# Kernel tuning notes

Hardware: AMD Instinct MI355X
Metric: run time of the kernel (lower is better)

The kernel has to match this reference:

```python
import jax, jax.numpy as jnp
import numpy as np

N = 100_000      # nodes
E = 1_600_000    # edges (before self loops)
IN, HID, OUT, H = 128, 32, 40, 4
NEG_SLOPE = 0.2  # PyG GATConv default


def setup_inputs() -> dict:
    key = jax.random.key(0)
    ks = jax.random.split(key, 10)
    s = 0.1  # small init scale (glorot-like)
    return {
        "x": jax.random.normal(ks[0], (N, IN), jnp.float32),
        "edge_index": jax.random.randint(ks[1], (2, E), 0, N, dtype=jnp.int32),
        "W1": jax.random.normal(ks[2], (IN, H * HID), jnp.float32) * s,
        "att_src1": jax.random.normal(ks[3], (H, HID), jnp.float32) * s,
        "att_dst1": jax.random.normal(ks[4], (H, HID), jnp.float32) * s,
        "b1": jnp.zeros((H * HID,), jnp.float32),
        "W2": jax.random.normal(ks[5], (H * HID, H * OUT), jnp.float32) * s,
        "att_src2": jax.random.normal(ks[6], (H, OUT), jnp.float32) * s,
        "att_dst2": jax.random.normal(ks[7], (H, OUT), jnp.float32) * s,
        "b2": jnp.zeros((OUT,), jnp.float32),
    }


def gat_layer(x, src, dst, W, a_src, a_dst, b, concat):
    """PyG-style GATConv: edge (src -> dst), softmax over incoming edges per dst."""
    Hh, C = a_src.shape
    h = (x @ W).reshape(-1, Hh, C)                      # [N, H, C]
    s_src = jnp.einsum('nhc,hc->nh', h, a_src)           # [N, H]
    s_dst = jnp.einsum('nhc,hc->nh', h, a_dst)           # [N, H]
    e = jax.nn.leaky_relu(s_src[src] + s_dst[dst], NEG_SLOPE)  # [E', H]
    m = jax.ops.segment_max(e, dst, num_segments=N)      # per-dst max for stability
    p = jnp.exp(e - m[dst])
    z = jax.ops.segment_sum(p, dst, num_segments=N)
    alpha = p / z[dst]                                    # segment softmax [E', H]
    out = jax.ops.segment_sum(alpha[:, :, None] * h[src], dst, num_segments=N)  # [N,H,C]
    out = out.reshape(-1, Hh * C) if concat else out.mean(axis=1)
    return out + b


def reference(x, edge_index, W1, att_src1, att_dst1, b1, W2, att_src2, att_dst2, b2):
    loops = jnp.arange(N, dtype=edge_index.dtype)        # PyG add_self_loops=True
    src = jnp.concatenate([edge_index[0], loops])
    dst = jnp.concatenate([edge_index[1], loops])
    h = jax.nn.elu(gat_layer(x, src, dst, W1, att_src1, att_dst1, b1, concat=True))
    h = gat_layer(h, src, dst, W2, att_src2, att_dst2, b2, concat=False)
    return jax.nn.log_softmax(h, axis=1)
```

## Files before the change

### kernel.cpp

```cpp
#include <hip/hip_runtime.h>
#include <hip/hip_bf16.h>

#define N_NODES 100000
#define M_PAD   100096
#define N_EDGES 1600000
#define E_TOT   (N_EDGES + N_NODES)
#define NEG_SLOPE 0.2f

#define G_NODES 128
#define BUCKETS ((N_NODES + G_NODES - 1) / G_NODES)
#define REP 512
#define SLICE ((E_TOT + REP - 1) / REP)

typedef __attribute__((ext_vector_type(8))) short s16x8;
typedef __attribute__((ext_vector_type(4))) float f32x4;
typedef __attribute__((ext_vector_type(2))) float f32x2;

__device__ __forceinline__ float lo16(unsigned u) { return __uint_as_float(u << 16); }
__device__ __forceinline__ float hi16(unsigned u) { return __uint_as_float(u & 0xffff0000u); }

__device__ __forceinline__ short f2bf(float f) {
    __hip_bfloat16 b = __float2bfloat16(f);
    return *(short*)&b;
}


__global__ __launch_bounds__(256) void slice_count_kernel(const int* __restrict__ ei,
                                                          int* __restrict__ cnt) {
    __shared__ int h[BUCKETS];
    for (int i = threadIdx.x; i < BUCKETS; i += 256) h[i] = 0;
    __syncthreads();
    int r = blockIdx.x;
    int lo = r * SLICE, hi = min(lo + SLICE, E_TOT);
    for (int e = lo + threadIdx.x; e < hi; e += 256) {
        int d = (e < N_EDGES) ? ei[N_EDGES + e] : e - N_EDGES;
        atomicAdd(&h[d >> 7], 1);
    }
    __syncthreads();
    for (int i = threadIdx.x; i < BUCKETS; i += 256)
        cnt[(size_t)r * BUCKETS + i] = h[i];
}

__global__ __launch_bounds__(REP) void col_scan_kernel(int* __restrict__ cnt,
                                                       int* __restrict__ bsum) {
    __shared__ int lds[REP];
    int b = blockIdx.x, tid = threadIdx.x;
    int v = cnt[(size_t)tid * BUCKETS + b];
    lds[tid] = v;
    __syncthreads();
    for (int off = 1; off < REP; off <<= 1) {
        int t = (tid >= off) ? lds[tid - off] : 0;
        __syncthreads();
        lds[tid] += t;
        __syncthreads();
    }
    cnt[(size_t)tid * BUCKETS + b] = lds[tid] - v;
    if (tid == REP - 1) bsum[b] = lds[tid];
}

__global__ __launch_bounds__(1024) void bucket_scan_kernel(const int* __restrict__ bsum,
                                                           int* __restrict__ boff) {
    __shared__ int lds[1024];
    int tid = threadIdx.x;
    int v = (tid < BUCKETS) ? bsum[tid] : 0;
    lds[tid] = v;
    __syncthreads();
    for (int off = 1; off < 1024; off <<= 1) {
        int t = (tid >= off) ? lds[tid - off] : 0;
        __syncthreads();
        lds[tid] += t;
        __syncthreads();
    }
    if (tid < BUCKETS) boff[tid] = lds[tid] - v;
    if (tid == 0) boff[BUCKETS] = E_TOT;
}

__global__ __launch_bounds__(256) void bucket_scatter_kernel(const int* __restrict__ ei,
                                                             const int* __restrict__ colx,
                                                             const int* __restrict__ boff,
                                                             int2* __restrict__ tmp) {
    __shared__ int lcur[BUCKETS];
    int r = blockIdx.x;
    for (int i = threadIdx.x; i < BUCKETS; i += 256)
        lcur[i] = boff[i] + colx[(size_t)r * BUCKETS + i];
    __syncthreads();
    int lo = r * SLICE, hi = min(lo + SLICE, E_TOT);
    for (int e = lo + threadIdx.x; e < hi; e += 256) {
        int s, d;
        if (e < N_EDGES) { s = ei[e]; d = ei[N_EDGES + e]; }
        else             { s = d = e - N_EDGES; }
        int pos = atomicAdd(&lcur[d >> 7], 1);
        tmp[pos] = make_int2(s, d);
    }
}

__global__ __launch_bounds__(256) void bucket_build_kernel(const int2* __restrict__ tmp,
                                                           const int* __restrict__ boff,
                                                           int* __restrict__ rowptr,
                                                           int* __restrict__ csr) {
    __shared__ int hcnt[G_NODES];
    __shared__ int hoff[G_NODES];
    int b = blockIdx.x;
    int base = boff[b], cnt = boff[b + 1] - base;
    int tid = threadIdx.x;
    if (tid < G_NODES) hcnt[tid] = 0;
    __syncthreads();
    for (int i = tid; i < cnt; i += 256)
        atomicAdd(&hcnt[tmp[base + i].y & (G_NODES - 1)], 1);
    __syncthreads();
    if (tid < G_NODES) hoff[tid] = hcnt[tid];
    __syncthreads();
    for (int off = 1; off < G_NODES; off <<= 1) {
        int t = (tid < G_NODES && tid >= off) ? hoff[tid - off] : 0;
        __syncthreads();
        if (tid < G_NODES) hoff[tid] += t;
        __syncthreads();
    }
    if (tid < G_NODES) {
        int excl = hoff[tid] - hcnt[tid];
        int node = b * G_NODES + tid;
        if (node < N_NODES) rowptr[node] = base + excl;
        hcnt[tid] = excl;
    }
    __syncthreads();
    for (int i = tid; i < cnt; i += 256) {
        int2 e = tmp[base + i];
        int pos = base + atomicAdd(&hcnt[e.y & (G_NODES - 1)], 1);
        csr[pos] = e.x;
    }
    if (b == 0 && tid == 0) rowptr[N_NODES] = E_TOT;
}


__global__ void cvt_w_kernel(const float* __restrict__ W1, __hip_bfloat16* __restrict__ W1t,
                             const float* __restrict__ W2, __hip_bfloat16* __restrict__ W2t) {
    int idx = blockIdx.x * blockDim.x + threadIdx.x;
    if (idx < 128 * 128) {
        int k = idx >> 7, n = idx & 127;
        W1t[n * 128 + k] = __float2bfloat16(W1[idx]);
    } else if (idx < 128 * 128 + 128 * 160) {
        int i = idx - 128 * 128;
        int k = i / 160, n = i - k * 160;
        W2t[n * 128 + k] = __float2bfloat16(W2[i]);
    }
}


template<int NCOLS>
__global__ __launch_bounds__(256) void mfma_gemm_f32a_kernel(const float* __restrict__ A,
                                                             const __hip_bfloat16* __restrict__ Bt,
                                                             unsigned char* __restrict__ Cq) {
    constexpr int CG = NCOLS / 32;
    int wid = threadIdx.x >> 6;
    int lane = threadIdx.x & 63;
    int wr = wid >> 1, wc = wid & 1;
    int l15 = lane & 15, lk = lane >> 4;

    s16x8 bfrag[CG][4];
    #pragma unroll
    for (int cg = 0; cg < CG; ++cg) {
        int col = wc * (NCOLS / 2) + cg * 16 + l15;
        #pragma unroll
        for (int ks = 0; ks < 4; ++ks)
            bfrag[cg][ks] = *(const s16x8*)&Bt[col * 128 + ks * 32 + lk * 8];
    }
    int rowblk = blockIdx.x * 128;
    #pragma unroll
    for (int st = 0; st < 4; ++st) {
        int rbase = rowblk + st * 32 + wr * 16;
        int row = rbase + l15;
        bool ok = row < N_NODES;
        s16x8 afrag[4];
        #pragma unroll
        for (int ks = 0; ks < 4; ++ks) {
            if (ok) {
                float4 a0 = *(const float4*)&A[(size_t)row * 128 + ks * 32 + lk * 8];
                float4 a1 = *(const float4*)&A[(size_t)row * 128 + ks * 32 + lk * 8 + 4];
                s16x8 af;
                af[0] = f2bf(a0.x); af[1] = f2bf(a0.y); af[2] = f2bf(a0.z); af[3] = f2bf(a0.w);
                af[4] = f2bf(a1.x); af[5] = f2bf(a1.y); af[6] = f2bf(a1.z); af[7] = f2bf(a1.w);
                afrag[ks] = af;
            } else {
                afrag[ks] = (s16x8){0,0,0,0,0,0,0,0};
            }
        }
        f32x4 acc[CG];
        #pragma unroll
        for (int cg = 0; cg < CG; ++cg) acc[cg] = (f32x4){0.f, 0.f, 0.f, 0.f};
        #pragma unroll
        for (int ks = 0; ks < 4; ++ks) {
            #pragma unroll
            for (int cg = 0; cg < CG; ++cg)
                acc[cg] = __builtin_amdgcn_mfma_f32_16x16x32_bf16(afrag[ks], bfrag[cg][ks], acc[cg], 0, 0, 0);
        }
        #pragma unroll
        for (int cg = 0; cg < CG; ++cg) {
            int c = wc * (NCOLS / 2) + cg * 16 + l15;
            unsigned w01 = __builtin_amdgcn_cvt_pk_fp8_f32(acc[cg][0], acc[cg][1], 0, false);
            unsigned w23 = __builtin_amdgcn_cvt_pk_fp8_f32(acc[cg][2], acc[cg][3], 0, false);
            size_t base = (size_t)(rbase + lk * 4) * NCOLS + c;
            Cq[base]             = (unsigned char)(w01 & 0xff);
            Cq[base + NCOLS]     = (unsigned char)((w01 >> 8) & 0xff);
            Cq[base + 2 * NCOLS] = (unsigned char)(w23 & 0xff);
            Cq[base + 3 * NCOLS] = (unsigned char)((w23 >> 8) & 0xff);
        }
    }
}


template<int NCOLS>
__global__ __launch_bounds__(256) void mfma_gemm_kernel(const __hip_bfloat16* __restrict__ A,
                                                        const __hip_bfloat16* __restrict__ Bt,
                                                        unsigned char* __restrict__ Cq) {
    constexpr int CG = NCOLS / 32;
    int wid = threadIdx.x >> 6;
    int lane = threadIdx.x & 63;
    int wr = wid >> 1, wc = wid & 1;
    int l15 = lane & 15, lk = lane >> 4;

    s16x8 bfrag[CG][4];
    #pragma unroll
    for (int cg = 0; cg < CG; ++cg) {
        int col = wc * (NCOLS / 2) + cg * 16 + l15;
        #pragma unroll
        for (int ks = 0; ks < 4; ++ks)
            bfrag[cg][ks] = *(const s16x8*)&Bt[col * 128 + ks * 32 + lk * 8];
    }
    int rowblk = blockIdx.x * 128;
    #pragma unroll
    for (int st = 0; st < 4; ++st) {
        int rbase = rowblk + st * 32 + wr * 16;
        s16x8 afrag[4];
        #pragma unroll
        for (int ks = 0; ks < 4; ++ks)
            afrag[ks] = *(const s16x8*)&A[(size_t)(rbase + l15) * 128 + ks * 32 + lk * 8];
        f32x4 acc[CG];
        #pragma unroll
        for (int cg = 0; cg < CG; ++cg) acc[cg] = (f32x4){0.f, 0.f, 0.f, 0.f};
        #pragma unroll
        for (int ks = 0; ks < 4; ++ks) {
            #pragma unroll
            for (int cg = 0; cg < CG; ++cg)
                acc[cg] = __builtin_amdgcn_mfma_f32_16x16x32_bf16(afrag[ks], bfrag[cg][ks], acc[cg], 0, 0, 0);
        }
        #pragma unroll
        for (int cg = 0; cg < CG; ++cg) {
            int c = wc * (NCOLS / 2) + cg * 16 + l15;
            unsigned w01 = __builtin_amdgcn_cvt_pk_fp8_f32(acc[cg][0], acc[cg][1], 0, false);
            unsigned w23 = __builtin_amdgcn_cvt_pk_fp8_f32(acc[cg][2], acc[cg][3], 0, false);
            size_t base = (size_t)(rbase + lk * 4) * NCOLS + c;
            Cq[base]             = (unsigned char)(w01 & 0xff);
            Cq[base + NCOLS]     = (unsigned char)((w01 >> 8) & 0xff);
            Cq[base + 2 * NCOLS] = (unsigned char)(w23 & 0xff);
            Cq[base + 3 * NCOLS] = (unsigned char)((w23 >> 8) & 0xff);
        }
    }
}


template<int C, int J>
__global__ void score_fp8_kernel(const unsigned char* __restrict__ hq,
                                 const float* __restrict__ att_src,
                                 const float* __restrict__ att_dst,
                                 float* __restrict__ s_src, float* __restrict__ s_dst, int n) {
    int idx = blockIdx.x * blockDim.x + threadIdx.x;
    if (idx >= n * 4) return;
    int node = idx >> 2, hd = idx & 3;
    const unsigned char* hp = hq + (size_t)node * J + hd * C;
    const float* as = att_src + hd * C;
    const float* ad = att_dst + hd * C;
    float ss = 0.f, sd = 0.f;
    #pragma unroll
    for (int c8 = 0; c8 < C / 8; ++c8) {
        uint2 u = *(const uint2*)&hp[c8 * 8];
        f32x2 v0 = __builtin_amdgcn_cvt_pk_f32_fp8(u.x, false);
        f32x2 v1 = __builtin_amdgcn_cvt_pk_f32_fp8(u.x, true);
        f32x2 v2 = __builtin_amdgcn_cvt_pk_f32_fp8(u.y, false);
        f32x2 v3 = __builtin_amdgcn_cvt_pk_f32_fp8(u.y, true);
        int c = c8 * 8;
        ss += v0.x * as[c]     + v0.y * as[c + 1] + v1.x * as[c + 2] + v1.y * as[c + 3]
            + v2.x * as[c + 4] + v2.y * as[c + 5] + v3.x * as[c + 6] + v3.y * as[c + 7];
        sd += v0.x * ad[c]     + v0.y * ad[c + 1] + v1.x * ad[c + 2] + v1.y * ad[c + 3]
            + v2.x * ad[c + 4] + v2.y * ad[c + 5] + v3.x * ad[c + 6] + v3.y * ad[c + 7];
    }
    s_src[idx] = ss;
    s_dst[idx] = sd;
}


__global__ __launch_bounds__(256) void agg1_kernel(
        const unsigned char* __restrict__ h1q, const float* __restrict__ s_src,
        const float* __restrict__ s_dst, const int* __restrict__ rowptr,
        const int* __restrict__ csr, const float* __restrict__ b1,
        __hip_bfloat16* __restrict__ out1) {
    int d = blockIdx.x * 4 + (threadIdx.x >> 6);
    if (d >= N_NODES) return;
    int lane = threadIdx.x & 63;
    int c0 = lane * 2;
    int hd = lane >> 4;
    float sdst = s_dst[d * 4 + hd];
    f32x2 acc = {0.f, 0.f};
    float z = 0.f;
    int beg = __builtin_amdgcn_readfirstlane(rowptr[d]);
    int end = __builtin_amdgcn_readfirstlane(rowptr[d + 1]);
    int j = beg;
    for (; j + 3 < end; j += 4) {
        #pragma unroll
        for (int t = 0; t < 4; ++t) {
            int s = __builtin_amdgcn_readfirstlane(csr[j + t]);
            const float* srow = s_src + (size_t)s * 4;
            const unsigned char* row = h1q + (size_t)s * 128;
            float e = srow[hd] + sdst;
            e = fmaxf(e, NEG_SLOPE * e);
            float q = __expf(e);
            unsigned u = *(const unsigned short*)&row[c0];
            f32x2 v = __builtin_amdgcn_cvt_pk_f32_fp8(u, false);
            f32x2 qq = {q, q};
            acc += qq * v;
            z += q;
        }
    }
    for (; j < end; ++j) {
        int s = __builtin_amdgcn_readfirstlane(csr[j]);
        const float* srow = s_src + (size_t)s * 4;
        const unsigned char* row = h1q + (size_t)s * 128;
        float e = srow[hd] + sdst;
        e = fmaxf(e, NEG_SLOPE * e);
        float q = __expf(e);
        unsigned u = *(const unsigned short*)&row[c0];
        f32x2 v = __builtin_amdgcn_cvt_pk_f32_fp8(u, false);
        f32x2 qq = {q, q};
        acc += qq * v;
        z += q;
    }
    float invz = 1.0f / z;
    float vx = acc.x * invz + b1[c0];
    float vy = acc.y * invz + b1[c0 + 1];
    vx = vx > 0.f ? vx : __expf(vx) - 1.0f;
    vy = vy > 0.f ? vy : __expf(vy) - 1.0f;
    __hip_bfloat162 o;
    o.x = __float2bfloat16(vx);
    o.y = __float2bfloat16(vy);
    *(__hip_bfloat162*)&out1[(size_t)d * 128 + c0] = o;
}


__global__ __launch_bounds__(256) void agg2_kernel(
        const unsigned char* __restrict__ h2q, const float* __restrict__ s_src,
        const float* __restrict__ s_dst, const int* __restrict__ rowptr,
        const int* __restrict__ csr, const float* __restrict__ b2,
        float* __restrict__ out) {
    int d = blockIdx.x * 4 + (threadIdx.x >> 6);
    if (d >= N_NODES) return;
    int lane = threadIdx.x & 63;
    int ll = lane < 40 ? lane : 39;
    int hd = ll / 10;
    int voff = ll * 4;
    float sdst = s_dst[d * 4 + hd];
    f32x2 acc01 = {0.f, 0.f}, acc23 = {0.f, 0.f};
    float z = 0.f;
    int beg = __builtin_amdgcn_readfirstlane(rowptr[d]);
    int end = __builtin_amdgcn_readfirstlane(rowptr[d + 1]);
    int j = beg;
    for (; j + 3 < end; j += 4) {
        #pragma unroll
        for (int t = 0; t < 4; ++t) {
            int s = __builtin_amdgcn_readfirstlane(csr[j + t]);
            const float* srow = s_src + (size_t)s * 4;
            const unsigned char* row = h2q + (size_t)s * 160;
            float e = srow[hd] + sdst;
            e = fmaxf(e, NEG_SLOPE * e);
            float q = __expf(e);
            unsigned u = *(const unsigned*)&row[voff];
            f32x2 v01 = __builtin_amdgcn_cvt_pk_f32_fp8(u, false);
            f32x2 v23 = __builtin_amdgcn_cvt_pk_f32_fp8(u, true);
            f32x2 qq = {q, q};
            acc01 += qq * v01;
            acc23 += qq * v23;
            z += q;
        }
    }
    for (; j < end; ++j) {
        int s = __builtin_amdgcn_readfirstlane(csr[j]);
        const float* srow = s_src + (size_t)s * 4;
        const unsigned char* row = h2q + (size_t)s * 160;
        float e = srow[hd] + sdst;
        e = fmaxf(e, NEG_SLOPE * e);
        float q = __expf(e);
        unsigned u = *(const unsigned*)&row[voff];
        f32x2 v01 = __builtin_amdgcn_cvt_pk_f32_fp8(u, false);
        f32x2 v23 = __builtin_amdgcn_cvt_pk_f32_fp8(u, true);
        f32x2 qq = {q, q};
        acc01 += qq * v01;
        acc23 += qq * v23;
        z += q;
    }
    float invz = 1.0f / z;
    float rx = acc01.x * invz, ry = acc01.y * invz;
    float rz = acc23.x * invz, rw = acc23.y * invz;
    float sx = rx + __shfl(rx, lane + 10) + __shfl(rx, lane + 20) + __shfl(rx, lane + 30);
    float sy = ry + __shfl(ry, lane + 10) + __shfl(ry, lane + 20) + __shfl(ry, lane + 30);
    float sz = rz + __shfl(rz, lane + 10) + __shfl(rz, lane + 20) + __shfl(rz, lane + 30);
    float sw = rw + __shfl(rw, lane + 10) + __shfl(rw, lane + 20) + __shfl(rw, lane + 30);
    int lc = lane < 10 ? lane : 9;
    float4 bb = *(const float4*)&b2[lc * 4];
    bool own = lane < 10;
    float vx = own ? sx * 0.25f + bb.x : -1e30f;
    float vy = own ? sy * 0.25f + bb.y : -1e30f;
    float vz = own ? sz * 0.25f + bb.z : -1e30f;
    float vw = own ? sw * 0.25f + bb.w : -1e30f;
    float m = fmaxf(fmaxf(vx, vy), fmaxf(vz, vw));
    #pragma unroll
    for (int off = 1; off < 16; off <<= 1) m = fmaxf(m, __shfl_xor(m, off));
    float ssum = 0.f;
    if (own) {
        ssum = __expf(vx - m) + __expf(vy - m) + __expf(vz - m) + __expf(vw - m);
    }
    #pragma unroll
    for (int off = 1; off < 16; off <<= 1) ssum += __shfl_xor(ssum, off);
    float lse = m + __logf(ssum);
    if (own) {
        float4 o = {vx - lse, vy - lse, vz - lse, vw - lse};
        *(float4*)&out[(size_t)d * 40 + lane * 4] = o;
    }
}


extern "C" void kernel_launch(void* const* d_in, const int* in_sizes, int n_in,
                              void* d_out, int out_size, void* d_ws, size_t ws_size,
                              hipStream_t stream) {
    const float* x   = (const float*)d_in[0];
    const int*   ei  = (const int*)d_in[1];
    const float* W1  = (const float*)d_in[2];
    const float* as1 = (const float*)d_in[3];
    const float* ad1 = (const float*)d_in[4];
    const float* b1  = (const float*)d_in[5];
    const float* W2  = (const float*)d_in[6];
    const float* as2 = (const float*)d_in[7];
    const float* ad2 = (const float*)d_in[8];
    const float* b2  = (const float*)d_in[9];
    float* out = (float*)d_out;

    char* ws = (char*)d_ws;
    size_t off = 0;
    auto alloc = [&](size_t bytes) {
        void* p = ws + off;
        off += (bytes + 255) & ~(size_t)255;
        return p;
    };
    unsigned char*  h1q   = (unsigned char*)alloc((size_t)M_PAD * 128);
    unsigned char*  h2q   = (unsigned char*)alloc((size_t)M_PAD * 160);
    __hip_bfloat16* out1b = (__hip_bfloat16*)alloc((size_t)M_PAD * 128 * 2);
    __hip_bfloat16* W1t   = (__hip_bfloat16*)alloc((size_t)128 * 128 * 2);
    __hip_bfloat16* W2t   = (__hip_bfloat16*)alloc((size_t)160 * 128 * 2);
    float* s_src1  = (float*)alloc((size_t)N_NODES * 4 * 4);
    float* s_dst1  = (float*)alloc((size_t)N_NODES * 4 * 4);
    float* s_src2  = (float*)alloc((size_t)N_NODES * 4 * 4);
    float* s_dst2  = (float*)alloc((size_t)N_NODES * 4 * 4);
    int2*  tmp     = (int2*)alloc((size_t)E_TOT * 8);
    int*   rowptr  = (int*)alloc((size_t)(N_NODES + 1) * 4);
    int*   csr     = (int*)alloc((size_t)E_TOT * 4);
    int*   cnt     = (int*)alloc((size_t)REP * BUCKETS * 4);
    int*   bsum    = (int*)alloc((size_t)BUCKETS * 4);
    int*   boff    = (int*)alloc((size_t)(BUCKETS + 1) * 4);

    slice_count_kernel<<<REP, 256, 0, stream>>>(ei, cnt);
    col_scan_kernel<<<BUCKETS, REP, 0, stream>>>(cnt, bsum);
    bucket_scan_kernel<<<1, 1024, 0, stream>>>(bsum, boff);
    bucket_scatter_kernel<<<REP, 256, 0, stream>>>(ei, cnt, boff, tmp);
    bucket_build_kernel<<<BUCKETS, 256, 0, stream>>>(tmp, boff, rowptr, csr);

    cvt_w_kernel<<<(128 * 128 + 128 * 160 + 255) / 256, 256, 0, stream>>>(W1, W1t, W2, W2t);

    mfma_gemm_f32a_kernel<128><<<M_PAD / 128, 256, 0, stream>>>(x, W1t, h1q);
    score_fp8_kernel<32, 128><<<(N_NODES * 4 + 255) / 256, 256, 0, stream>>>(h1q, as1, ad1, s_src1, s_dst1, N_NODES);
    agg1_kernel<<<(N_NODES + 3) / 4, 256, 0, stream>>>(h1q, s_src1, s_dst1, rowptr, csr, b1, out1b);

    mfma_gemm_kernel<160><<<M_PAD / 128, 256, 0, stream>>>(out1b, W2t, h2q);
    score_fp8_kernel<40, 160><<<(N_NODES * 4 + 255) / 256, 256, 0, stream>>>(h2q, as2, ad2, s_src2, s_dst2, N_NODES);
    agg2_kernel<<<(N_NODES + 3) / 4, 256, 0, stream>>>(h2q, s_src2, s_dst2, rowptr, csr, b2, out);
}
```

Before: 259.2 us.

## Pack bucket temp edges into one int and batch attention exp across lanes

The bucket scatter now stores each edge as a single packed int (source shifted left by 7 bits, low 7 bits of the destination) instead of an int2, halving the temp buffer traffic in the scatter and build kernels. In both aggregation kernels, each wave now computes the leaky-relu and exp scores for 8 edges by 4 heads in parallel across lanes, then broadcasts them with ds_bpermute. This removes the per-lane redundant exp and s_src loads in the inner loop. The loop now always processes groups of 8 edges and masks the tail with zero weights, so it does some wasted work on partial groups and adds LDS-permute latency.

```diff
diff --git a/kernel.cpp b/kernel.cpp
--- a/kernel.cpp
+++ b/kernel.cpp
@@ -78,7 +78,7 @@
 __global__ __launch_bounds__(256) void bucket_scatter_kernel(const int* __restrict__ ei,
                                                              const int* __restrict__ colx,
                                                              const int* __restrict__ boff,
-                                                             int2* __restrict__ tmp) {
+                                                             int* __restrict__ tmp) {
     __shared__ int lcur[BUCKETS];
     int r = blockIdx.x;
     for (int i = threadIdx.x; i < BUCKETS; i += 256)
@@ -90,11 +90,11 @@
         if (e < N_EDGES) { s = ei[e]; d = ei[N_EDGES + e]; }
         else             { s = d = e - N_EDGES; }
         int pos = atomicAdd(&lcur[d >> 7], 1);
-        tmp[pos] = make_int2(s, d);
-    }
-}
-
-__global__ __launch_bounds__(256) void bucket_build_kernel(const int2* __restrict__ tmp,
+        tmp[pos] = (s << 7) | (d & (G_NODES - 1));
+    }
+}
+
+__global__ __launch_bounds__(256) void bucket_build_kernel(const int* __restrict__ tmp,
                                                            const int* __restrict__ boff,
                                                            int* __restrict__ rowptr,
                                                            int* __restrict__ csr) {
@@ -106,7 +106,7 @@
     if (tid < G_NODES) hcnt[tid] = 0;
     __syncthreads();
     for (int i = tid; i < cnt; i += 256)
-        atomicAdd(&hcnt[tmp[base + i].y & (G_NODES - 1)], 1);
+        atomicAdd(&hcnt[tmp[base + i] & (G_NODES - 1)], 1);
     __syncthreads();
     if (tid < G_NODES) hoff[tid] = hcnt[tid];
     __syncthreads();
@@ -124,9 +124,9 @@
     }
     __syncthreads();
     for (int i = tid; i < cnt; i += 256) {
-        int2 e = tmp[base + i];
-        int pos = base + atomicAdd(&hcnt[e.y & (G_NODES - 1)], 1);
-        csr[pos] = e.x;
+        int v = tmp[base + i];
+        int pos = base + atomicAdd(&hcnt[v & (G_NODES - 1)], 1);
+        csr[pos] = v >> 7;
     }
     if (b == 0 && tid == 0) rowptr[N_NODES] = E_TOT;
 }
@@ -298,40 +298,31 @@
     int lane = threadIdx.x & 63;
     int c0 = lane * 2;
     int hd = lane >> 4;
-    float sdst = s_dst[d * 4 + hd];
+    int bp = hd << 2;
+    int eg = (lane >> 2) & 7;
+    float sdall = s_dst[d * 4 + (lane & 3)];
     f32x2 acc = {0.f, 0.f};
     float z = 0.f;
     int beg = __builtin_amdgcn_readfirstlane(rowptr[d]);
     int end = __builtin_amdgcn_readfirstlane(rowptr[d + 1]);
-    int j = beg;
-    for (; j + 3 < end; j += 4) {
-        #pragma unroll
-        for (int t = 0; t < 4; ++t) {
-            int s = __builtin_amdgcn_readfirstlane(csr[j + t]);
-            const float* srow = s_src + (size_t)s * 4;
+    for (int j = beg; j < end; j += 8) {
+        int cnt = end - j;
+        int se = csr[min(j + eg, end - 1)];
+        float ee = s_src[(size_t)se * 4 + (lane & 3)] + sdall;
+        ee = fmaxf(ee, NEG_SLOPE * ee);
+        float qv = (eg < cnt) ? __expf(ee) : 0.f;
+        int qbits = __float_as_int(qv);
+        #pragma unroll
+        for (int t = 0; t < 8; ++t) {
+            float q = __int_as_float(__builtin_amdgcn_ds_bpermute(bp + t * 16, qbits));
+            int s = __builtin_amdgcn_readfirstlane(csr[min(j + t, end - 1)]);
             const unsigned char* row = h1q + (size_t)s * 128;
-            float e = srow[hd] + sdst;
-            e = fmaxf(e, NEG_SLOPE * e);
-            float q = __expf(e);
             unsigned u = *(const unsigned short*)&row[c0];
             f32x2 v = __builtin_amdgcn_cvt_pk_f32_fp8(u, false);
             f32x2 qq = {q, q};
             acc += qq * v;
             z += q;
         }
-    }
-    for (; j < end; ++j) {
-        int s = __builtin_amdgcn_readfirstlane(csr[j]);
-        const float* srow = s_src + (size_t)s * 4;
-        const unsigned char* row = h1q + (size_t)s * 128;
-        float e = srow[hd] + sdst;
-        e = fmaxf(e, NEG_SLOPE * e);
-        float q = __expf(e);
-        unsigned u = *(const unsigned short*)&row[c0];
-        f32x2 v = __builtin_amdgcn_cvt_pk_f32_fp8(u, false);
-        f32x2 qq = {q, q};
-        acc += qq * v;
-        z += q;
     }
     float invz = 1.0f / z;
     float vx = acc.x * invz + b1[c0];
@@ -355,22 +346,26 @@
     int lane = threadIdx.x & 63;
     int ll = lane < 40 ? lane : 39;
     int hd = ll / 10;
+    int bp = hd << 2;
+    int eg = (lane >> 2) & 7;
     int voff = ll * 4;
-    float sdst = s_dst[d * 4 + hd];
+    float sdall = s_dst[d * 4 + (lane & 3)];
     f32x2 acc01 = {0.f, 0.f}, acc23 = {0.f, 0.f};
     float z = 0.f;
     int beg = __builtin_amdgcn_readfirstlane(rowptr[d]);
     int end = __builtin_amdgcn_readfirstlane(rowptr[d + 1]);
-    int j = beg;
-    for (; j + 3 < end; j += 4) {
-        #pragma unroll
-        for (int t = 0; t < 4; ++t) {
-            int s = __builtin_amdgcn_readfirstlane(csr[j + t]);
-            const float* srow = s_src + (size_t)s * 4;
+    for (int j = beg; j < end; j += 8) {
+        int cnt = end - j;
+        int se = csr[min(j + eg, end - 1)];
+        float ee = s_src[(size_t)se * 4 + (lane & 3)] + sdall;
+        ee = fmaxf(ee, NEG_SLOPE * ee);
+        float qv = (eg < cnt) ? __expf(ee) : 0.f;
+        int qbits = __float_as_int(qv);
+        #pragma unroll
+        for (int t = 0; t < 8; ++t) {
+            float q = __int_as_float(__builtin_amdgcn_ds_bpermute(bp + t * 16, qbits));
+            int s = __builtin_amdgcn_readfirstlane(csr[min(j + t, end - 1)]);
             const unsigned char* row = h2q + (size_t)s * 160;
-            float e = srow[hd] + sdst;
-            e = fmaxf(e, NEG_SLOPE * e);
-            float q = __expf(e);
             unsigned u = *(const unsigned*)&row[voff];
             f32x2 v01 = __builtin_amdgcn_cvt_pk_f32_fp8(u, false);
             f32x2 v23 = __builtin_amdgcn_cvt_pk_f32_fp8(u, true);
@@ -379,21 +374,6 @@
             acc23 += qq * v23;
             z += q;
         }
-    }
-    for (; j < end; ++j) {
-        int s = __builtin_amdgcn_readfirstlane(csr[j]);
-        const float* srow = s_src + (size_t)s * 4;
-        const unsigned char* row = h2q + (size_t)s * 160;
-        float e = srow[hd] + sdst;
-        e = fmaxf(e, NEG_SLOPE * e);
-        float q = __expf(e);
-        unsigned u = *(const unsigned*)&row[voff];
-        f32x2 v01 = __builtin_amdgcn_cvt_pk_f32_fp8(u, false);
-        f32x2 v23 = __builtin_amdgcn_cvt_pk_f32_fp8(u, true);
-        f32x2 qq = {q, q};
-        acc01 += qq * v01;
-        acc23 += qq * v23;
-        z += q;
     }
     float invz = 1.0f / z;
     float rx = acc01.x * invz, ry = acc01.y * invz;
@@ -457,7 +437,7 @@
     float* s_dst1  = (float*)alloc((size_t)N_NODES * 4 * 4);
     float* s_src2  = (float*)alloc((size_t)N_NODES * 4 * 4);
     float* s_dst2  = (float*)alloc((size_t)N_NODES * 4 * 4);
-    int2*  tmp     = (int2*)alloc((size_t)E_TOT * 8);
+    int*   tmp     = (int*)alloc((size_t)E_TOT * 4);
     int*   rowptr  = (int*)alloc((size_t)(N_NODES + 1) * 4);
     int*   csr     = (int*)alloc((size_t)E_TOT * 4);
     int*   cnt     = (int*)alloc((size_t)REP * BUCKETS * 4);
```

Result: faster. 249.9 us (-3.6%).
